# Kernel optimization log

Measured on AMD Instinct MI355X. Metric: run time of the kernel, lower is better.

Reference implementation:

```python
import jax, jax.numpy as jnp
import numpy as np

N = 4096
IN_DIM = 128
OUT_DIM = 64
LEAKY_SLOPE = 0.2


def setup_inputs() -> dict:
    key = jax.random.key(0)
    ks = jax.random.split(key, 8)
    H = jax.random.normal(ks[0], (N, IN_DIM), dtype=jnp.float32)
    # dense 0/1 adjacency per relation (int constants w.r.t. autodiff)
    A_buys = jax.random.randint(ks[1], (N, N), 0, 2, dtype=jnp.int32)
    A_views = jax.random.randint(ks[2], (N, N), 0, 2, dtype=jnp.int32)
    # xavier_uniform for W (stored [in, out]; Wh = H @ W == torch Linear with weight W.T)
    s_w = float(np.sqrt(6.0 / (IN_DIM + OUT_DIM)))
    W_buys = jax.random.uniform(ks[3], (IN_DIM, OUT_DIM), jnp.float32, -s_w, s_w)
    W_views = jax.random.uniform(ks[4], (IN_DIM, OUT_DIM), jnp.float32, -s_w, s_w)
    # xavier_uniform on a.view(1, 2*out_dim)
    s_a = float(np.sqrt(6.0 / (1 + 2 * OUT_DIM)))
    a_buys = jax.random.uniform(ks[5], (2 * OUT_DIM,), jnp.float32, -s_a, s_a)
    a_views = jax.random.uniform(ks[6], (2 * OUT_DIM,), jnp.float32, -s_a, s_a)
    bias = jnp.zeros((OUT_DIM,), dtype=jnp.float32)
    return {"H": H, "A_buys": A_buys, "A_views": A_views,
            "W_buys": W_buys, "W_views": W_views,
            "a_buys": a_buys, "a_views": a_views, "bias": bias}


def _relation(H, A, W, a):
    Wh = H @ W                                  # [N, OUT]
    # (cat(Wh_i, Wh_j) * a).sum(-1) == Wh_i @ a[:OUT] + Wh_j @ a[OUT:]
    s_i = Wh @ a[:OUT_DIM]                      # [N]
    s_j = Wh @ a[OUT_DIM:]                      # [N]
    e = jax.nn.leaky_relu(s_i[:, None] + s_j[None, :], LEAKY_SLOPE)  # [N, N]
    e = jnp.where(A == 0, -jnp.inf, e)
    alpha = jnp.nan_to_num(jax.nn.softmax(e, axis=1))                # isolated rows -> 0
    return alpha @ Wh                           # [N, OUT]


def reference(H, A_buys, A_views, W_buys, W_views, a_buys, a_views, bias):
    agg = _relation(H, A_buys, W_buys, a_buys) + _relation(H, A_views, W_views, a_views)
    return agg + bias
```

## Files before the change

kernel.cpp:

```cpp
#include <hip/hip_runtime.h>

#define NN 4096
#define IND 128
#define OUTD 64
#define WJ 128
#define NWIN 8
#define LOG2E 1.44269504088896340736f

typedef __attribute__((ext_vector_type(4))) float  floatx4;
typedef __attribute__((ext_vector_type(8))) __bf16 bf16x8;
typedef __attribute__((ext_vector_type(4))) int    intx4;

#if __has_builtin(__builtin_amdgcn_exp2f)
#define EXP2(x) __builtin_amdgcn_exp2f(x)
#else
#define EXP2(x) exp2f(x)
#endif

__device__ __forceinline__ unsigned short f2bf(float f) {
  unsigned int u = __float_as_uint(f);
  u += 0x7fffu + ((u >> 16) & 1u);
  return (unsigned short)(u >> 16);
}

__global__ __launch_bounds__(256) void gat_prep(
    const float* __restrict__ H,
    const float* __restrict__ W0, const float* __restrict__ W1,
    const float* __restrict__ av0, const float* __restrict__ av1,
    unsigned short* __restrict__ whF,
    float* __restrict__ sA, float* __restrict__ sB)
{
  const int rel = blockIdx.y;
  const float* __restrict__ W  = rel ? W1 : W0;
  const float* __restrict__ av = rel ? av1 : av0;
  const int i0 = blockIdx.x * 16;
  const int t = threadIdx.x;
  const int c = t & 63;
  const int wv = __builtin_amdgcn_readfirstlane(t >> 6);
  const float* __restrict__ hp = H + (size_t)(i0 + wv * 4) * IND;

  float acc0 = 0.f, acc1 = 0.f, acc2 = 0.f, acc3 = 0.f;
#pragma unroll 8
  for (int k = 0; k < IND; k += 4) {
    float4 h0 = *(const float4*)(hp + k);
    float4 h1 = *(const float4*)(hp + IND + k);
    float4 h2 = *(const float4*)(hp + 2 * IND + k);
    float4 h3 = *(const float4*)(hp + 3 * IND + k);
    float w0 = W[(k + 0) * OUTD + c];
    float w1 = W[(k + 1) * OUTD + c];
    float w2 = W[(k + 2) * OUTD + c];
    float w3 = W[(k + 3) * OUTD + c];
    acc0 += h0.x * w0 + h0.y * w1 + h0.z * w2 + h0.w * w3;
    acc1 += h1.x * w0 + h1.y * w1 + h1.z * w2 + h1.w * w3;
    acc2 += h2.x * w0 + h2.y * w1 + h2.z * w2 + h2.w * w3;
    acc3 += h3.x * w0 + h3.y * w1 + h3.z * w2 + h3.w * w3;
  }

  const float alo = av[c] * LOG2E, ahi = av[OUTD + c] * LOG2E;
  float pa0 = acc0 * alo, pa1 = acc1 * alo, pa2 = acc2 * alo, pa3 = acc3 * alo;
  float pb0 = acc0 * ahi, pb1 = acc1 * ahi, pb2 = acc2 * ahi, pb3 = acc3 * ahi;
#pragma unroll
  for (int off = 32; off >= 1; off >>= 1) {
    pa0 += __shfl_xor(pa0, off); pa1 += __shfl_xor(pa1, off);
    pa2 += __shfl_xor(pa2, off); pa3 += __shfl_xor(pa3, off);
    pb0 += __shfl_xor(pb0, off); pb1 += __shfl_xor(pb1, off);
    pb2 += __shfl_xor(pb2, off); pb3 += __shfl_xor(pb3, off);
  }
  const int ibase = i0 + wv * 4;
  if (c == 0) {
    float* sa = sA + rel * NN + ibase;
    float* sb = sB + rel * NN + ibase;
    sa[0] = pa0; sa[1] = pa1; sa[2] = pa2; sa[3] = pa3;
    sb[0] = pb0; sb[1] = pb1; sb[2] = pb2; sb[3] = pb3;
  }

  unsigned long long packed =
      (unsigned long long)f2bf(acc0)        | ((unsigned long long)f2bf(acc1) << 16) |
      ((unsigned long long)f2bf(acc2) << 32) | ((unsigned long long)f2bf(acc3) << 48);
  *(unsigned long long*)(whF + ((size_t)(rel * 512 + (ibase >> 3)) * 64 + c) * 8 + (ibase & 7)) = packed;
}

__global__ __launch_bounds__(256, 2) void gat_fused(
    const int* __restrict__ A0, const int* __restrict__ A1,
    const unsigned short* __restrict__ whF,
    const float* __restrict__ sA, const float* __restrict__ sB,
    float* __restrict__ numer,
    float* __restrict__ denom)
{
  __shared__ char lds[4][2][4096];
  const int rel  = blockIdx.y;
  const int i0   = blockIdx.x * 16;
  const int t    = threadIdx.x;
  const int w    = t >> 6;
  const int lane = t & 63;
  const int quad = lane >> 4;
  const int m    = lane & 15;
  const int lj   = lane & 31;
  const int half = lane >> 5;
  const int s_st = lj >> 1;
  const int wboff = s_st * 256 + (lj & 1) * 8;
  const int* __restrict__ A = rel ? A1 : A0;
  const unsigned short* __restrict__ wh = whF + (size_t)rel * 512 * 64 * 8;
  const float* __restrict__ sbp = sB + rel * NN;

  float si_r[8];
#pragma unroll
  for (int p = 0; p < 8; p++) si_r[p] = sA[rel * NN + i0 + 2 * p + half];

  const int jbase = w * (NWIN * WJ);

  floatx4 acc0 = {0.f,0.f,0.f,0.f}, acc1 = acc0, acc2 = acc0, acc3 = acc0, acc4 = acc0;
  bf16x8 vone;
#pragma unroll
  for (int k = 0; k < 8; k++) vone[k] = (__bf16)1.0f;

  intx4  av2[2][8];
  float4 sjv2[2];
  bf16x8 b[4][4];

  auto issueA = [&](int win) {
    const int jw = jbase + win * WJ;
    const int buf = win & 1;
    sjv2[buf] = *(const float4*)(sbp + jw + lj * 4);
    const int* pA = A + (size_t)(i0 + half) * NN + jw + lj * 4;
#pragma unroll
    for (int p = 0; p < 8; p++)
      av2[buf][p] = __builtin_nontemporal_load((const intx4*)(pA + (size_t)(2 * p) * NN));
  };

  auto stage = [&](int win) {
    const int buf = win & 1;
    char* slice = lds[w][buf];
    const float4 sjv = sjv2[buf];
#pragma unroll
    for (int p = 0; p < 8; p++) {
      const int rp = 2 * p + half;
      const float si = si_r[p];
      float t0 = si + sjv.x, t1 = si + sjv.y, t2 = si + sjv.z, t3 = si + sjv.w;
      float e0 = EXP2(fmaxf(t0, 0.2f * t0));
      float e1 = EXP2(fmaxf(t1, 0.2f * t1));
      float e2 = EXP2(fmaxf(t2, 0.2f * t2));
      float e3 = EXP2(fmaxf(t3, 0.2f * t3));
      const intx4 a4 = av2[buf][p];
      e0 = a4[0] ? e0 : 0.f;
      e1 = a4[1] ? e1 : 0.f;
      e2 = a4[2] ? e2 : 0.f;
      e3 = a4[3] ? e3 : 0.f;
      uint2 pk;
      pk.x = (unsigned)f2bf(e0) | ((unsigned)f2bf(e1) << 16);
      pk.y = (unsigned)f2bf(e2) | ((unsigned)f2bf(e3) << 16);
      *(uint2*)(slice + wboff + ((rp ^ s_st) & 15) * 16) = pk;
    }
  };

  auto issueB = [&](int win) {
    const int jw = jbase + win * WJ;
    const unsigned short* bb = wh + ((size_t)(jw >> 3) + quad) * 512 + (size_t)m * 8;
#pragma unroll
    for (int ks = 0; ks < 4; ks++)
#pragma unroll
      for (int nt = 0; nt < 4; nt++)
        b[ks][nt] = *(const bf16x8*)(bb + (size_t)ks * 2048 + nt * 128);
  };

  auto domfma = [&](int win) {
    char* slice = lds[w][win & 1];
    bf16x8 afr[4];
#pragma unroll
    for (int ks = 0; ks < 4; ks++) {
      const int s = ks * 4 + quad;
      afr[ks] = *(const bf16x8*)(slice + s * 256 + ((m ^ s) & 15) * 16);
    }
#pragma unroll
    for (int ks = 0; ks < 4; ks++) {
      acc0 = __builtin_amdgcn_mfma_f32_16x16x32_bf16(afr[ks], b[ks][0], acc0, 0, 0, 0);
      acc1 = __builtin_amdgcn_mfma_f32_16x16x32_bf16(afr[ks], b[ks][1], acc1, 0, 0, 0);
      acc2 = __builtin_amdgcn_mfma_f32_16x16x32_bf16(afr[ks], b[ks][2], acc2, 0, 0, 0);
      acc3 = __builtin_amdgcn_mfma_f32_16x16x32_bf16(afr[ks], b[ks][3], acc3, 0, 0, 0);
      acc4 = __builtin_amdgcn_mfma_f32_16x16x32_bf16(afr[ks], vone,     acc4, 0, 0, 0);
    }
  };

  issueA(0);
  stage(0);
  issueA(1);

#pragma unroll
  for (int win = 0; win < NWIN; win++) {
    issueB(win);
    if (win + 2 < NWIN) issueA(win + 2);
    if (win + 1 < NWIN) stage(win + 1);
    domfma(win);
  }

  float* redw  = (float*)lds[w][0];
  float* dredw = (float*)lds[w][1];
#pragma unroll
  for (int r = 0; r < 4; r++) {
    const int row = quad * 4 + r;
    redw[row * 64 + 0 * 16 + m] = acc0[r];
    redw[row * 64 + 1 * 16 + m] = acc1[r];
    redw[row * 64 + 2 * 16 + m] = acc2[r];
    redw[row * 64 + 3 * 16 + m] = acc3[r];
  }
  if (m == 0) {
#pragma unroll
    for (int r = 0; r < 4; r++) dredw[quad * 4 + r] = acc4[r];
  }
  __syncthreads();

  const int c  = t & 63;
  const int r0 = t >> 6;
  const size_t base = (size_t)rel * NN;
#pragma unroll
  for (int rr = r0; rr < 16; rr += 4) {
    float nsum = 0.f, ds = 0.f;
#pragma unroll
    for (int ww = 0; ww < 4; ww++) {
      nsum += ((const float*)lds[ww][0])[rr * 64 + c];
      ds   += ((const float*)lds[ww][1])[rr];
    }
    numer[(base + i0 + rr) * OUTD + c] = nsum;
    if (c == 0) denom[base + i0 + rr] = ds;
  }
}

__global__ __launch_bounds__(256) void gat_combine(
    const float* __restrict__ numer, const float* __restrict__ denom,
    const float* __restrict__ bias, float* __restrict__ out)
{
  const int idx = blockIdx.x * 256 + threadIdx.x;
  const int i  = idx >> 4;
  const int c4 = idx & 15;
  const float4* nv = (const float4*)numer;

  float4 o = ((const float4*)bias)[c4];
#pragma unroll
  for (int rel = 0; rel < 2; rel++) {
    const size_t base = (size_t)rel * NN + i;
    float4 n = nv[base * 16 + c4];
    float  d = denom[base];
    float inv = d > 0.f ? 1.f / d : 0.f;
    o.x += n.x * inv; o.y += n.y * inv; o.z += n.z * inv; o.w += n.w * inv;
  }
  ((float4*)out)[idx] = o;
}

extern "C" void kernel_launch(void* const* d_in, const int* in_sizes, int n_in,
                              void* d_out, int out_size, void* d_ws, size_t ws_size,
                              hipStream_t stream) {
  const float* H    = (const float*)d_in[0];
  const int*   A0   = (const int*)d_in[1];
  const int*   A1   = (const int*)d_in[2];
  const float* W0   = (const float*)d_in[3];
  const float* W1   = (const float*)d_in[4];
  const float* av0  = (const float*)d_in[5];
  const float* av1  = (const float*)d_in[6];
  const float* bias = (const float*)d_in[7];
  float* out = (float*)d_out;

  const size_t whF_b = (size_t)2 * 512 * 64 * 8 * 2;
  const size_t s_b   = (size_t)2 * NN * 4;

  unsigned short* whF   = (unsigned short*)d_ws;
  float*          sA    = (float*)((char*)d_ws + whF_b);
  float*          sB    = (float*)((char*)d_ws + whF_b + s_b);
  float*          numer = (float*)((char*)d_ws + whF_b + 2 * s_b);
  float*          denom = numer + (size_t)2 * NN * OUTD;

  gat_prep<<<dim3(NN / 16, 2), 256, 0, stream>>>(H, W0, W1, av0, av1, whF, sA, sB);
  gat_fused<<<dim3(NN / 16, 2), 256, 0, stream>>>(A0, A1, whF, sA, sB, numer, denom);
  gat_combine<<<(NN * OUTD / 4) / 256, 256, 0, stream>>>(numer, denom, bias, out);
}
```

Measured before the change: 178.0 us.

## Fuse both relations and combine step into one 512-thread attention kernel

Each block now handles both relations for its 16 rows using 8 waves, with each wave covering 512 columns instead of 1024. The block normalises and sums the two relations and adds bias directly into the output. This removes the numer/denom workspace round trip and the separate combine launch, at the cost of twice as many accumulator registers per wave and a 512-thread block with 64KB of LDS, which may reduce occupancy. The grid also shrinks from 512 blocks to 256.

```diff
diff --git a/kernel.cpp b/kernel.cpp
--- a/kernel.cpp
+++ b/kernel.cpp
@@ -4,7 +4,7 @@
 #define IND 128
 #define OUTD 64
 #define WJ 128
-#define NWIN 8
+#define NWIN 4
 #define LOG2E 1.44269504088896340736f
 
 typedef __attribute__((ext_vector_type(4))) float  floatx4;
@@ -80,15 +80,14 @@
   *(unsigned long long*)(whF + ((size_t)(rel * 512 + (ibase >> 3)) * 64 + c) * 8 + (ibase & 7)) = packed;
 }
 
-__global__ __launch_bounds__(256, 2) void gat_fused(
+__global__ __launch_bounds__(512, 2) void gat_fused(
     const int* __restrict__ A0, const int* __restrict__ A1,
     const unsigned short* __restrict__ whF,
     const float* __restrict__ sA, const float* __restrict__ sB,
-    float* __restrict__ numer,
-    float* __restrict__ denom)
+    const float* __restrict__ bias,
+    float* __restrict__ out)
 {
-  __shared__ char lds[4][2][4096];
-  const int rel  = blockIdx.y;
+  __shared__ char lds[8][2][4096];
   const int i0   = blockIdx.x * 16;
   const int t    = threadIdx.x;
   const int w    = t >> 6;
@@ -99,151 +98,149 @@
   const int half = lane >> 5;
   const int s_st = lj >> 1;
   const int wboff = s_st * 256 + (lj & 1) * 8;
-  const int* __restrict__ A = rel ? A1 : A0;
-  const unsigned short* __restrict__ wh = whF + (size_t)rel * 512 * 64 * 8;
-  const float* __restrict__ sbp = sB + rel * NN;
-
-  float si_r[8];
-#pragma unroll
-  for (int p = 0; p < 8; p++) si_r[p] = sA[rel * NN + i0 + 2 * p + half];
-
   const int jbase = w * (NWIN * WJ);
 
-  floatx4 acc0 = {0.f,0.f,0.f,0.f}, acc1 = acc0, acc2 = acc0, acc3 = acc0, acc4 = acc0;
+  floatx4 acc[2][5];
+#pragma unroll
+  for (int r2 = 0; r2 < 2; r2++)
+#pragma unroll
+    for (int k = 0; k < 5; k++) acc[r2][k] = (floatx4){0.f, 0.f, 0.f, 0.f};
   bf16x8 vone;
 #pragma unroll
   for (int k = 0; k < 8; k++) vone[k] = (__bf16)1.0f;
 
-  intx4  av2[2][8];
-  float4 sjv2[2];
-  bf16x8 b[4][4];
-
-  auto issueA = [&](int win) {
-    const int jw = jbase + win * WJ;
-    const int buf = win & 1;
-    sjv2[buf] = *(const float4*)(sbp + jw + lj * 4);
-    const int* pA = A + (size_t)(i0 + half) * NN + jw + lj * 4;
-#pragma unroll
-    for (int p = 0; p < 8; p++)
-      av2[buf][p] = __builtin_nontemporal_load((const intx4*)(pA + (size_t)(2 * p) * NN));
-  };
-
-  auto stage = [&](int win) {
-    const int buf = win & 1;
-    char* slice = lds[w][buf];
-    const float4 sjv = sjv2[buf];
-#pragma unroll
-    for (int p = 0; p < 8; p++) {
-      const int rp = 2 * p + half;
-      const float si = si_r[p];
-      float t0 = si + sjv.x, t1 = si + sjv.y, t2 = si + sjv.z, t3 = si + sjv.w;
-      float e0 = EXP2(fmaxf(t0, 0.2f * t0));
-      float e1 = EXP2(fmaxf(t1, 0.2f * t1));
-      float e2 = EXP2(fmaxf(t2, 0.2f * t2));
-      float e3 = EXP2(fmaxf(t3, 0.2f * t3));
-      const intx4 a4 = av2[buf][p];
-      e0 = a4[0] ? e0 : 0.f;
-      e1 = a4[1] ? e1 : 0.f;
-      e2 = a4[2] ? e2 : 0.f;
-      e3 = a4[3] ? e3 : 0.f;
-      uint2 pk;
-      pk.x = (unsigned)f2bf(e0) | ((unsigned)f2bf(e1) << 16);
-      pk.y = (unsigned)f2bf(e2) | ((unsigned)f2bf(e3) << 16);
-      *(uint2*)(slice + wboff + ((rp ^ s_st) & 15) * 16) = pk;
-    }
-  };
-
-  auto issueB = [&](int win) {
-    const int jw = jbase + win * WJ;
-    const unsigned short* bb = wh + ((size_t)(jw >> 3) + quad) * 512 + (size_t)m * 8;
-#pragma unroll
-    for (int ks = 0; ks < 4; ks++)
-#pragma unroll
-      for (int nt = 0; nt < 4; nt++)
-        b[ks][nt] = *(const bf16x8*)(bb + (size_t)ks * 2048 + nt * 128);
-  };
-
-  auto domfma = [&](int win) {
-    char* slice = lds[w][win & 1];
-    bf16x8 afr[4];
-#pragma unroll
-    for (int ks = 0; ks < 4; ks++) {
-      const int s = ks * 4 + quad;
-      afr[ks] = *(const bf16x8*)(slice + s * 256 + ((m ^ s) & 15) * 16);
-    }
-#pragma unroll
-    for (int ks = 0; ks < 4; ks++) {
-      acc0 = __builtin_amdgcn_mfma_f32_16x16x32_bf16(afr[ks], b[ks][0], acc0, 0, 0, 0);
-      acc1 = __builtin_amdgcn_mfma_f32_16x16x32_bf16(afr[ks], b[ks][1], acc1, 0, 0, 0);
-      acc2 = __builtin_amdgcn_mfma_f32_16x16x32_bf16(afr[ks], b[ks][2], acc2, 0, 0, 0);
-      acc3 = __builtin_amdgcn_mfma_f32_16x16x32_bf16(afr[ks], b[ks][3], acc3, 0, 0, 0);
-      acc4 = __builtin_amdgcn_mfma_f32_16x16x32_bf16(afr[ks], vone,     acc4, 0, 0, 0);
-    }
-  };
-
-  issueA(0);
-  stage(0);
-  issueA(1);
-
-#pragma unroll
-  for (int win = 0; win < NWIN; win++) {
-    issueB(win);
-    if (win + 2 < NWIN) issueA(win + 2);
-    if (win + 1 < NWIN) stage(win + 1);
-    domfma(win);
-  }
-
-  float* redw  = (float*)lds[w][0];
-  float* dredw = (float*)lds[w][1];
-#pragma unroll
-  for (int r = 0; r < 4; r++) {
-    const int row = quad * 4 + r;
-    redw[row * 64 + 0 * 16 + m] = acc0[r];
-    redw[row * 64 + 1 * 16 + m] = acc1[r];
-    redw[row * 64 + 2 * 16 + m] = acc2[r];
-    redw[row * 64 + 3 * 16 + m] = acc3[r];
-  }
-  if (m == 0) {
-#pragma unroll
-    for (int r = 0; r < 4; r++) dredw[quad * 4 + r] = acc4[r];
-  }
-  __syncthreads();
+#pragma unroll
+  for (int rel = 0; rel < 2; rel++) {
+    const int* __restrict__ A = rel ? A1 : A0;
+    const unsigned short* __restrict__ wh = whF + (size_t)rel * 512 * 64 * 8;
+    const float* __restrict__ sbp = sB + rel * NN;
+
+    float si_r[8];
+#pragma unroll
+    for (int p = 0; p < 8; p++) si_r[p] = sA[rel * NN + i0 + 2 * p + half];
+
+    intx4  av2[2][8];
+    float4 sjv2[2];
+    bf16x8 b[4][4];
+
+    auto issueA = [&](int win) {
+      const int jw = jbase + win * WJ;
+      const int buf = win & 1;
+      sjv2[buf] = *(const float4*)(sbp + jw + lj * 4);
+      const int* pA = A + (size_t)(i0 + half) * NN + jw + lj * 4;
+#pragma unroll
+      for (int p = 0; p < 8; p++)
+        av2[buf][p] = __builtin_nontemporal_load((const intx4*)(pA + (size_t)(2 * p) * NN));
+    };
+
+    auto stage = [&](int win) {
+      const int buf = win & 1;
+      char* slice = lds[w][buf];
+      const float4 sjv = sjv2[buf];
+#pragma unroll
+      for (int p = 0; p < 8; p++) {
+        const int rp = 2 * p + half;
+        const float si = si_r[p];
+        float t0 = si + sjv.x, t1 = si + sjv.y, t2 = si + sjv.z, t3 = si + sjv.w;
+        float e0 = EXP2(fmaxf(t0, 0.2f * t0));
+        float e1 = EXP2(fmaxf(t1, 0.2f * t1));
+        float e2 = EXP2(fmaxf(t2, 0.2f * t2));
+        float e3 = EXP2(fmaxf(t3, 0.2f * t3));
+        const intx4 a4 = av2[buf][p];
+        e0 = a4[0] ? e0 : 0.f;
+        e1 = a4[1] ? e1 : 0.f;
+        e2 = a4[2] ? e2 : 0.f;
+        e3 = a4[3] ? e3 : 0.f;
+        uint2 pk;
+        pk.x = (unsigned)f2bf(e0) | ((unsigned)f2bf(e1) << 16);
+        pk.y = (unsigned)f2bf(e2) | ((unsigned)f2bf(e3) << 16);
+        *(uint2*)(slice + wboff + ((rp ^ s_st) & 15) * 16) = pk;
+      }
+    };
+
+    auto issueB = [&](int win) {
+      const int jw = jbase + win * WJ;
+      const unsigned short* bb = wh + ((size_t)(jw >> 3) + quad) * 512 + (size_t)m * 8;
+#pragma unroll
+      for (int ks = 0; ks < 4; ks++)
+#pragma unroll
+        for (int nt = 0; nt < 4; nt++)
+          b[ks][nt] = *(const bf16x8*)(bb + (size_t)ks * 2048 + nt * 128);
+    };
+
+    auto domfma = [&](int win) {
+      char* slice = lds[w][win & 1];
+      bf16x8 afr[4];
+#pragma unroll
+      for (int ks = 0; ks < 4; ks++) {
+        const int s = ks * 4 + quad;
+        afr[ks] = *(const bf16x8*)(slice + s * 256 + ((m ^ s) & 15) * 16);
+      }
+#pragma unroll
+      for (int ks = 0; ks < 4; ks++) {
+        acc[rel][0] = __builtin_amdgcn_mfma_f32_16x16x32_bf16(afr[ks], b[ks][0], acc[rel][0], 0, 0, 0);
+        acc[rel][1] = __builtin_amdgcn_mfma_f32_16x16x32_bf16(afr[ks], b[ks][1], acc[rel][1], 0, 0, 0);
+        acc[rel][2] = __builtin_amdgcn_mfma_f32_16x16x32_bf16(afr[ks], b[ks][2], acc[rel][2], 0, 0, 0);
+        acc[rel][3] = __builtin_amdgcn_mfma_f32_16x16x32_bf16(afr[ks], b[ks][3], acc[rel][3], 0, 0, 0);
+        acc[rel][4] = __builtin_amdgcn_mfma_f32_16x16x32_bf16(afr[ks], vone,     acc[rel][4], 0, 0, 0);
+      }
+    };
+
+    issueA(0);
+    stage(0);
+    issueA(1);
+#pragma unroll
+    for (int win = 0; win < NWIN; win++) {
+      issueB(win);
+      if (win + 2 < NWIN) issueA(win + 2);
+      if (win + 1 < NWIN) stage(win + 1);
+      domfma(win);
+    }
+  }
 
   const int c  = t & 63;
   const int r0 = t >> 6;
-  const size_t base = (size_t)rel * NN;
-#pragma unroll
-  for (int rr = r0; rr < 16; rr += 4) {
-    float nsum = 0.f, ds = 0.f;
-#pragma unroll
-    for (int ww = 0; ww < 4; ww++) {
-      nsum += ((const float*)lds[ww][0])[rr * 64 + c];
-      ds   += ((const float*)lds[ww][1])[rr];
-    }
-    numer[(base + i0 + rr) * OUTD + c] = nsum;
-    if (c == 0) denom[base + i0 + rr] = ds;
-  }
-}
-
-__global__ __launch_bounds__(256) void gat_combine(
-    const float* __restrict__ numer, const float* __restrict__ denom,
-    const float* __restrict__ bias, float* __restrict__ out)
-{
-  const int idx = blockIdx.x * 256 + threadIdx.x;
-  const int i  = idx >> 4;
-  const int c4 = idx & 15;
-  const float4* nv = (const float4*)numer;
-
-  float4 o = ((const float4*)bias)[c4];
+  float nacc[2][2], dacc[2][2];
+
 #pragma unroll
   for (int rel = 0; rel < 2; rel++) {
-    const size_t base = (size_t)rel * NN + i;
-    float4 n = nv[base * 16 + c4];
-    float  d = denom[base];
-    float inv = d > 0.f ? 1.f / d : 0.f;
-    o.x += n.x * inv; o.y += n.y * inv; o.z += n.z * inv; o.w += n.w * inv;
-  }
-  ((float4*)out)[idx] = o;
+    __syncthreads();
+    float* redw  = (float*)lds[w][0];
+    float* dredw = (float*)lds[w][1];
+#pragma unroll
+    for (int r = 0; r < 4; r++) {
+      const int row = quad * 4 + r;
+      redw[row * 64 + 0 * 16 + m] = acc[rel][0][r];
+      redw[row * 64 + 1 * 16 + m] = acc[rel][1][r];
+      redw[row * 64 + 2 * 16 + m] = acc[rel][2][r];
+      redw[row * 64 + 3 * 16 + m] = acc[rel][3][r];
+    }
+    if (m == 0) {
+#pragma unroll
+      for (int r = 0; r < 4; r++) dredw[quad * 4 + r] = acc[rel][4][r];
+    }
+    __syncthreads();
+#pragma unroll
+    for (int k = 0; k < 2; k++) {
+      const int rr = r0 + k * 8;
+      float nsum = 0.f, ds = 0.f;
+#pragma unroll
+      for (int ww = 0; ww < 8; ww++) {
+        nsum += ((const float*)lds[ww][0])[rr * 64 + c];
+        ds   += ((const float*)lds[ww][1])[rr];
+      }
+      nacc[rel][k] = nsum; dacc[rel][k] = ds;
+    }
+  }
+
+  const float bv = bias[c];
+#pragma unroll
+  for (int k = 0; k < 2; k++) {
+    const int rr = r0 + k * 8;
+    float inv0 = dacc[0][k] > 0.f ? 1.f / dacc[0][k] : 0.f;
+    float inv1 = dacc[1][k] > 0.f ? 1.f / dacc[1][k] : 0.f;
+    out[(size_t)(i0 + rr) * OUTD + c] = nacc[0][k] * inv0 + nacc[1][k] * inv1 + bv;
+  }
 }
 
 extern "C" void kernel_launch(void* const* d_in, const int* in_sizes, int n_in,
@@ -262,13 +259,10 @@
   const size_t whF_b = (size_t)2 * 512 * 64 * 8 * 2;
   const size_t s_b   = (size_t)2 * NN * 4;
 
-  unsigned short* whF   = (unsigned short*)d_ws;
-  float*          sA    = (float*)((char*)d_ws + whF_b);
-  float*          sB    = (float*)((char*)d_ws + whF_b + s_b);
-  float*          numer = (float*)((char*)d_ws + whF_b + 2 * s_b);
-  float*          denom = numer + (size_t)2 * NN * OUTD;
+  unsigned short* whF = (unsigned short*)d_ws;
+  float*          sA  = (float*)((char*)d_ws + whF_b);
+  float*          sB  = (float*)((char*)d_ws + whF_b + s_b);
 
   gat_prep<<<dim3(NN / 16, 2), 256, 0, stream>>>(H, W0, W1, av0, av1, whF, sA, sB);
-  gat_fused<<<dim3(NN / 16, 2), 256, 0, stream>>>(A0, A1, whF, sA, sB, numer, denom);
-  gat_combine<<<(NN * OUTD / 4) / 256, 256, 0, stream>>>(numer, denom, bias, out);
-}
+  gat_fused<<<NN / 16, 512, 0, stream>>>(A0, A1, whF, sA, sB, bias, out);
+}
```

New measurement: 178.2 us. Within noise of the previous version (+0.1%).
